# Optimization experiments

Measured on AMD Instinct MI355X. Metric: run time of the kernel, lower is better.

The kernel has to match this reference:

```python
import jax, jax.numpy as jnp
import numpy as np

B, L, D, N_NODE = 1024, 32, 128, 50000

def setup_inputs() -> dict:
    key = jax.random.key(0)
    ks = jax.random.split(key, 20)
    rn = lambda k, shape, s=0.05: (jax.random.normal(k, shape, jnp.float32) * s)
    return {
        "items": jax.random.randint(ks[0], (B, L), 0, N_NODE),
        "A_in": jax.random.uniform(ks[1], (B, L, L), jnp.float32),
        "A_out": jax.random.uniform(ks[2], (B, L, L), jnp.float32),
        "inter_item_emb": jax.random.normal(ks[3], (B, L, D), jnp.float32),
        "seq_len": jax.random.randint(ks[4], (B,), 1, L + 1),
        "emb_table": rn(ks[5], (N_NODE, D), 0.1),
        # GGNN propagation weights
        "W_in": rn(ks[6], (D, D)), "b_in": jnp.zeros((D,), jnp.float32),
        "W_out": rn(ks[7], (D, D)), "b_out": jnp.zeros((D,), jnp.float32),
        "W_a": rn(ks[8], (2 * D, 3 * D)),   # acts on concat(a_in, a_out)
        "U_h": rn(ks[9], (D, 3 * D)),       # acts on hidden state
        "b_gru": jnp.zeros((3 * D,), jnp.float32),
        # ItemFusing GRUCell (input=local/intra, hidden=global/inter)
        "Wi": rn(ks[10], (D, 3 * D)), "bi": jnp.zeros((3 * D,), jnp.float32),
        "Wh": rn(ks[11], (D, 3 * D)), "bh": jnp.zeros((3 * D,), jnp.float32),
        # get_final_s attention readout
        "W1": rn(ks[12], (D, D)), "b1": jnp.zeros((D,), jnp.float32),
        "W2": rn(ks[13], (D, D)), "b2": jnp.zeros((D,), jnp.float32),
        "wq": rn(ks[14], (D, 1)), "bq": jnp.zeros((1,), jnp.float32),
        "W3": rn(ks[15], (2 * D, D)), "b3": jnp.zeros((D,), jnp.float32),
    }

def _gru_gates(gi, gh, h_prev):
    # torch GRU(Cell) math: r,z,n gate order
    i_r, i_z, i_n = jnp.split(gi, 3, axis=-1)
    h_r, h_z, h_n = jnp.split(gh, 3, axis=-1)
    r = jax.nn.sigmoid(i_r + h_r)
    z = jax.nn.sigmoid(i_z + h_z)
    n = jnp.tanh(i_n + r * h_n)
    return (1.0 - z) * n + z * h_prev

def reference(items, A_in, A_out, inter_item_emb, seq_len, emb_table,
              W_in, b_in, W_out, b_out, W_a, U_h, b_gru,
              Wi, bi, Wh, bh, W1, b1, W2, b2, wq, bq, W3, b3):
    # --- embedding lookup: [B, L, D]
    h = emb_table[items]
    # --- GGNN propagation (1 step): adjacency matmul + GRU-gated update
    a_in = jnp.einsum('blm,bmd->bld', A_in, h @ W_in + b_in)
    a_out = jnp.einsum('blm,bmd->bld', A_out, h @ W_out + b_out)
    a = jnp.concatenate([a_in, a_out], axis=-1)          # [B, L, 2D]
    intra = _gru_gates(a @ W_a + b_gru, h @ U_h, h)       # [B, L, D]
    # --- ItemFusing: GRUCell(input=intra, hidden=inter)
    final = _gru_gates(intra @ Wi + bi, inter_item_emb @ Wh + bh, inter_item_emb)
    # --- get_final_s (session attention readout, padded/masked form)
    mask = (jnp.arange(L)[None, :] < seq_len[:, None]).astype(final.dtype)  # [B, L]
    v_n = final[jnp.arange(B), seq_len - 1]                                 # [B, D] last valid node
    gates = jax.nn.sigmoid((v_n @ W1 + b1)[:, None, :] + final @ W2 + b2)   # [B, L, D]
    alpha = gates @ wq + bq                                                 # [B, L, 1]
    s_g = jnp.sum(alpha * final * mask[:, :, None], axis=1)                 # [B, D]
    h_s = jnp.concatenate([v_n, s_g], axis=-1) @ W3 + b3                    # [B, D]
    # --- Embedding2Score (item_fusing branch): final_s @ emb.T
    scores = h_s @ emb_table.T                                              # [B, N_NODE]
    return scores
```

## Files before the change

kernel.cpp:

```cpp
#include <hip/hip_runtime.h>
#include <hip/hip_bf16.h>

#define L_SEQ 32
#define DIM 128
#define NN 50000

typedef __attribute__((ext_vector_type(8))) short bf16x8s;
typedef __attribute__((ext_vector_type(4))) float f32x4;

__device__ __forceinline__ float bf2f(short s){
    union{unsigned u; float f;} v; v.u = ((unsigned)(unsigned short)s) << 16; return v.f;
}
__device__ __forceinline__ short f2bf(float x){
    union{__hip_bfloat16 h; short s;} u; u.h = __float2bfloat16(x); return u.s;
}
__device__ __forceinline__ void ldf8(const float* p, float* w){
    const float4 a = *reinterpret_cast<const float4*>(p);
    const float4 b = *reinterpret_cast<const float4*>(p+4);
    w[0]=a.x; w[1]=a.y; w[2]=a.z; w[3]=a.w;
    w[4]=b.x; w[5]=b.y; w[6]=b.z; w[7]=b.w;
}
__device__ __forceinline__ void st8bf(short* dst, const float* v){
    union{ short s[8]; uint4 q; } u;
    #pragma unroll
    for (int i=0;i<8;++i) u.s[i] = f2bf(v[i]);
    *reinterpret_cast<uint4*>(dst) = u.q;
}
__device__ __forceinline__ bf16x8s cvt8(const float* v){
    union{ short s[8]; bf16x8s b; } u;
    #pragma unroll
    for (int i=0;i<8;++i) u.s[i] = f2bf(v[i]);
    return u.b;
}
__device__ __forceinline__ float sigmoidf(float x){ return 1.0f/(1.0f+__expf(-x)); }
__device__ __forceinline__ float tanh_fast(float x){
    x = fminf(fmaxf(x, -15.f), 15.f);
    float e = __expf(2.f*x);
    return (e-1.f)/(e+1.f);
}
__device__ __forceinline__ f32x4 mfma16(bf16x8s a, bf16x8s b, f32x4 c){
    return __builtin_amdgcn_mfma_f32_16x16x32_bf16(a, b, c, 0, 0, 0);
}

__global__ __launch_bounds__(256)
void prep_kernel(const float* __restrict__ W_in, const float* __restrict__ W_out,
                 const float* __restrict__ W_a,  const float* __restrict__ U_h,
                 const float* __restrict__ Wi,   const float* __restrict__ Wh,
                 const float* __restrict__ W1,   const float* __restrict__ W2,
                 const float* __restrict__ W3,   short* __restrict__ wt,
                 const float* __restrict__ emb,  short* __restrict__ embf)
{
    const int blk = blockIdx.x;
    if (blk < 1344) {
        int idx = blk*256 + threadIdx.x;
        const float* src; int Rm1, lR, C, local, off;
        if      (idx < 16384) { src=W_in;  local=idx;        off=0;      Rm1=127; lR=7; C=128; }
        else if (idx < 32768) { src=W_out; local=idx-16384;  off=16384;  Rm1=127; lR=7; C=128; }
        else if (idx < 131072){ src=W_a;   local=idx-32768;  off=32768;  Rm1=255; lR=8; C=384; }
        else if (idx < 180224){ src=U_h;   local=idx-131072; off=131072; Rm1=127; lR=7; C=384; }
        else if (idx < 229376){ src=Wi;    local=idx-180224; off=180224; Rm1=127; lR=7; C=384; }
        else if (idx < 278528){ src=Wh;    local=idx-229376; off=229376; Rm1=127; lR=7; C=384; }
        else if (idx < 294912){ src=W1;    local=idx-278528; off=278528; Rm1=127; lR=7; C=128; }
        else if (idx < 311296){ src=W2;    local=idx-294912; off=294912; Rm1=127; lR=7; C=128; }
        else if (idx < 344064){ src=W3;    local=idx-311296; off=311296; Rm1=255; lR=8; C=128; }
        else return;
        int r = local & Rm1;
        int c = local >> lR;
        wt[off + local] = f2bf(src[r*C + c]);
    } else {
        const size_t idx = ((size_t)(blk-1344)*256 + threadIdx.x) * 8;
        float v[8]; ldf8(emb + idx, v);
        st8bf(embf + idx, v);
    }
}

#define LDH 136
#define LDA 264
#define LDT 40

__global__ __launch_bounds__(256)
void graph_fused(const int* __restrict__ items,
                 const float* __restrict__ A_in, const float* __restrict__ A_out,
                 const float* __restrict__ inter,
                 const int* __restrict__ seq_len,
                 const float* __restrict__ emb,
                 const short* __restrict__ embf,
                 const float* __restrict__ b_in, const float* __restrict__ b_out,
                 const float* __restrict__ b_gru,
                 const float* __restrict__ bi, const float* __restrict__ bh,
                 const float* __restrict__ b1, const float* __restrict__ b2,
                 const float* __restrict__ wq, const float* __restrict__ bq,
                 const float* __restrict__ b3,
                 const short* __restrict__ wt,
                 short* __restrict__ hs_bf)
{
    const short* WinT  = wt + 0;
    const short* WoutT = wt + 16384;
    const short* WaT   = wt + 32768;
    const short* UhT   = wt + 131072;
    const short* WiT   = wt + 180224;
    const short* WhT   = wt + 229376;
    const short* W1T   = wt + 278528;
    const short* W2T   = wt + 294912;
    const short* W3T   = wt + 311296;

    __shared__ __align__(16) short s_h[32*LDH];
    __shared__ __align__(16) short s_a[32*LDA];
    __shared__ __align__(16) short s_r3[32*LDH];
    __shared__ __align__(16) short s_r4[2*32*LDH];

    short* s_Ain  = s_r3;
    short* s_Aout = s_r3 + 32*LDT;
    short* s_x    = s_r3;
    short* xT     = s_r4;
    short* s_int  = s_r4;
    short* s_fin  = s_r4 + 32*LDH;
    float* s_vn    = (float*)s_a;
    float* s_q1    = s_vn + 128;
    float* s_sg    = s_q1 + 128;
    float* s_red   = s_sg + 128;
    float* s_alpha = s_red + 256;

    const int b    = blockIdx.x;
    const int t    = threadIdx.x;
    const int wave = t >> 6;
    const int lane = t & 63;
    const int quad = lane >> 4;
    const int lc   = lane & 15;
    const int kq   = quad * 8;

    float pre_i[2][8];
    #pragma unroll
    for (int i=0;i<2;++i) {
        int c = t + i*256;
        int l = c >> 4, k = (c & 15) * 8;
        ldf8(inter + ((size_t)b*L_SEQ + l)*DIM + k, pre_i[i]);
    }
    if (embf) {
        #pragma unroll
        for (int i=0;i<2;++i) {
            int c = t + i*256;
            int l = c >> 4, k = (c & 15) * 8;
            int it = items[b*L_SEQ + l];
            *reinterpret_cast<uint4*>(&s_h[l*LDH + k]) =
                *reinterpret_cast<const uint4*>(embf + (size_t)it*DIM + k);
        }
    } else {
        #pragma unroll
        for (int i=0;i<2;++i) {
            int c = t + i*256;
            int l = c >> 4, k = (c & 15) * 8;
            int it = items[b*L_SEQ + l];
            float v[8]; ldf8(emb + (size_t)it*DIM + k, v);
            st8bf(&s_h[l*LDH + k], v);
        }
    }
    {
        const int which = t >> 7;
        const int rem   = t & 127;
        const int l = rem >> 2, m = (rem & 3) * 8;
        const float* src = which ? A_out : A_in;
        float v[8]; ldf8(src + b*L_SEQ*L_SEQ + l*L_SEQ + m, v);
        st8bf((which ? s_Aout : s_Ain) + l*LDT + m, v);
    }
    __syncthreads();

    #pragma unroll
    for (int op = 0; op < 2; ++op) {
        const short* WT_ = op ? WoutT : WinT;
        #pragma unroll
        for (int p = 0; p < 2; ++p) {
            const int nt = wave*2 + p;
            const int n  = nt*16 + lc;
            const float bv = op ? b_out[n] : b_in[n];
            f32x4 acc0 = {bv,bv,bv,bv}, acc1 = {bv,bv,bv,bv};
            #pragma unroll
            for (int ks = 0; ks < 4; ++ks) {
                const int ko = ks*32 + kq;
                bf16x8s bb = *(const bf16x8s*)(WT_ + n*128 + ko);
                bf16x8s a0 = *(const bf16x8s*)(&s_h[(lc   )*LDH + ko]);
                bf16x8s a1 = *(const bf16x8s*)(&s_h[(16+lc)*LDH + ko]);
                acc0 = mfma16(a0, bb, acc0);
                acc1 = mfma16(a1, bb, acc1);
            }
            union{short s[4]; unsigned long long q;} u0, u1;
            #pragma unroll
            for (int i=0;i<4;++i){ u0.s[i]=f2bf(acc0[i]); u1.s[i]=f2bf(acc1[i]); }
            *(unsigned long long*)(&xT[n*LDT + 0  + quad*4]) = u0.q;
            *(unsigned long long*)(&xT[n*LDT + 16 + quad*4]) = u1.q;
        }
        __syncthreads();
        const short* Abuf = op ? s_Aout : s_Ain;
        #pragma unroll
        for (int u = 0; u < 4; ++u) {
            int unit = wave*4 + u;
            int nt = unit >> 1, m0 = (unit & 1)*16;
            bf16x8s a  = *(const bf16x8s*)(&Abuf[(m0+lc)*LDT + kq]);
            bf16x8s bb = *(const bf16x8s*)(&xT[(nt*16+lc)*LDT + kq]);
            f32x4 acc = {0.f,0.f,0.f,0.f};
            acc = mfma16(a, bb, acc);
            #pragma unroll
            for (int i=0;i<4;++i)
                s_a[(m0+quad*4+i)*LDA + op*128 + nt*16 + lc] = f2bf(acc[i]);
        }
        __syncthreads();
    }

    #pragma unroll
    for (int i=0;i<2;++i) {
        int c = t + i*256;
        int l = c >> 4, k = (c & 15) * 8;
        st8bf(&s_int[l*LDH + k], pre_i[i]);
    }

    #pragma unroll
    for (int g = wave; g < 8; g += 4) {
        const int n = g*16 + lc;
        const float vr = b_gru[n], vz = b_gru[128+n], vn2 = b_gru[256+n];
        f32x4 ar[2], az[2], an[2], pr[2], pz[2], pn[2];
        #pragma unroll
        for (int m=0;m<2;++m){
            ar[m]=(f32x4){vr,vr,vr,vr}; az[m]=(f32x4){vz,vz,vz,vz}; an[m]=(f32x4){vn2,vn2,vn2,vn2};
            pr[m]=(f32x4){0,0,0,0}; pz[m]=pr[m]; pn[m]=pr[m];
        }
        #pragma unroll
        for (int ks=0; ks<8; ++ks) {
            const int ko = ks*32 + kq;
            bf16x8s br = *(const bf16x8s*)(WaT + (n      )*256 + ko);
            bf16x8s bz = *(const bf16x8s*)(WaT + (n + 128)*256 + ko);
            bf16x8s bn = *(const bf16x8s*)(WaT + (n + 256)*256 + ko);
            #pragma unroll
            for (int m=0;m<2;++m){
                bf16x8s a = *(const bf16x8s*)(&s_a[(m*16+lc)*LDA + ko]);
                ar[m]=mfma16(a,br,ar[m]); az[m]=mfma16(a,bz,az[m]); an[m]=mfma16(a,bn,an[m]);
            }
        }
        #pragma unroll
        for (int ks=0; ks<4; ++ks) {
            const int ko = ks*32 + kq;
            bf16x8s br = *(const bf16x8s*)(UhT + (n      )*128 + ko);
            bf16x8s bz = *(const bf16x8s*)(UhT + (n + 128)*128 + ko);
            bf16x8s bn = *(const bf16x8s*)(UhT + (n + 256)*128 + ko);
            #pragma unroll
            for (int m=0;m<2;++m){
                bf16x8s a = *(const bf16x8s*)(&s_h[(m*16+lc)*LDH + ko]);
                pr[m]=mfma16(a,br,pr[m]); pz[m]=mfma16(a,bz,pz[m]); pn[m]=mfma16(a,bn,pn[m]);
            }
        }
        #pragma unroll
        for (int m=0;m<2;++m)
        #pragma unroll
        for (int i=0;i<4;++i){
            const int row = m*16 + quad*4 + i;
            float hp = bf2f(s_h[row*LDH + n]);
            float r  = sigmoidf(ar[m][i] + pr[m][i]);
            float z  = sigmoidf(az[m][i] + pz[m][i]);
            float nn = tanh_fast(an[m][i] + r*pn[m][i]);
            s_x[row*LDH + n] = f2bf((1.f - z)*nn + z*hp);
        }
    }
    __syncthreads();

    #pragma unroll
    for (int g = wave; g < 8; g += 4) {
        const int n = g*16 + lc;
        const float vir = bi[n], viz = bi[128+n], vin = bi[256+n];
        const float vhr = bh[n], vhz = bh[128+n], vhn = bh[256+n];
        f32x4 ar[2], az[2], an[2], pr[2], pz[2], pn[2];
        #pragma unroll
        for (int m=0;m<2;++m){
            ar[m]=(f32x4){vir,vir,vir,vir}; az[m]=(f32x4){viz,viz,viz,viz}; an[m]=(f32x4){vin,vin,vin,vin};
            pr[m]=(f32x4){vhr,vhr,vhr,vhr}; pz[m]=(f32x4){vhz,vhz,vhz,vhz}; pn[m]=(f32x4){vhn,vhn,vhn,vhn};
        }
        #pragma unroll
        for (int ks=0; ks<4; ++ks) {
            const int ko = ks*32 + kq;
            bf16x8s br = *(const bf16x8s*)(WiT + (n      )*128 + ko);
            bf16x8s bz = *(const bf16x8s*)(WiT + (n + 128)*128 + ko);
            bf16x8s bn = *(const bf16x8s*)(WiT + (n + 256)*128 + ko);
            #pragma unroll
            for (int m=0;m<2;++m){
                bf16x8s a = *(const bf16x8s*)(&s_x[(m*16+lc)*LDH + ko]);
                ar[m]=mfma16(a,br,ar[m]); az[m]=mfma16(a,bz,az[m]); an[m]=mfma16(a,bn,an[m]);
            }
        }
        #pragma unroll
        for (int ks=0; ks<4; ++ks) {
            const int ko = ks*32 + kq;
            bf16x8s br = *(const bf16x8s*)(WhT + (n      )*128 + ko);
            bf16x8s bz = *(const bf16x8s*)(WhT + (n + 128)*128 + ko);
            bf16x8s bn = *(const bf16x8s*)(WhT + (n + 256)*128 + ko);
            #pragma unroll
            for (int m=0;m<2;++m){
                bf16x8s a = *(const bf16x8s*)(&s_int[(m*16+lc)*LDH + ko]);
                pr[m]=mfma16(a,br,pr[m]); pz[m]=mfma16(a,bz,pz[m]); pn[m]=mfma16(a,bn,pn[m]);
            }
        }
        #pragma unroll
        for (int m=0;m<2;++m)
        #pragma unroll
        for (int i=0;i<4;++i){
            const int row = m*16 + quad*4 + i;
            float hp = bf2f(s_int[row*LDH + n]);
            float r  = sigmoidf(ar[m][i] + pr[m][i]);
            float z  = sigmoidf(az[m][i] + pz[m][i]);
            float nn = tanh_fast(an[m][i] + r*pn[m][i]);
            s_fin[row*LDH + n] = f2bf((1.f - z)*nn + z*hp);
        }
    }
    __syncthreads();

    const int slen = seq_len[b];
    if (t < DIM) s_vn[t] = bf2f(s_fin[(slen-1)*LDH + t]);
    __syncthreads();
    if (t < DIM) {
        float acc = b1[t] + b2[t];
        #pragma unroll
        for (int k8=0; k8<16; ++k8) {
            union{ uint4 q; short s[8]; } u;
            u.q = *reinterpret_cast<const uint4*>(W1T + t*128 + k8*8);
            #pragma unroll
            for (int u2=0;u2<8;++u2) acc += s_vn[k8*8+u2]*bf2f(u.s[u2]);
        }
        s_q1[t] = acc;
    }
    __syncthreads();
    #pragma unroll
    for (int tl = wave; tl < 16; tl += 4) {
        const int m0 = (tl & 1)*16, nt = tl >> 1;
        const int n  = nt*16 + lc;
        f32x4 acc = {0.f,0.f,0.f,0.f};
        #pragma unroll
        for (int ks=0; ks<4; ++ks) {
            const int ko = ks*32 + kq;
            bf16x8s a  = *(const bf16x8s*)(&s_fin[(m0+lc)*LDH + ko]);
            bf16x8s bb = *(const bf16x8s*)(W2T + n*128 + ko);
            acc = mfma16(a, bb, acc);
        }
        const float qb  = s_q1[n];
        const float wqv = wq[n];
        float p[4];
        #pragma unroll
        for (int i=0;i<4;++i) p[i] = sigmoidf(acc[i] + qb) * wqv;
        #pragma unroll
        for (int off=1; off<16; off<<=1) {
            #pragma unroll
            for (int i=0;i<4;++i) p[i] += __shfl_xor(p[i], off);
        }
        if (lc == 0) {
            #pragma unroll
            for (int i=0;i<4;++i) s_red[(m0+quad*4+i)*8 + nt] = p[i];
        }
    }
    __syncthreads();
    if (t < L_SEQ) {
        float al = bq[0];
        #pragma unroll
        for (int u=0;u<8;++u) al += s_red[t*8+u];
        s_alpha[t] = (t < slen) ? al : 0.f;
    }
    __syncthreads();
    if (t < DIM) {
        float sg = 0.f;
        #pragma unroll
        for (int l=0;l<L_SEQ;++l) sg += s_alpha[l]*bf2f(s_fin[l*LDH + t]);
        s_sg[t] = sg;
    }
    __syncthreads();
    if (t < DIM) {
        float acc = b3[t];
        #pragma unroll
        for (int k8=0; k8<16; ++k8) {
            union{ uint4 q; short s[8]; } u;
            u.q = *reinterpret_cast<const uint4*>(W3T + t*256 + k8*8);
            #pragma unroll
            for (int u2=0;u2<8;++u2) acc += s_vn[k8*8+u2]*bf2f(u.s[u2]);
        }
        #pragma unroll
        for (int k8=0; k8<16; ++k8) {
            union{ uint4 q; short s[8]; } u;
            u.q = *reinterpret_cast<const uint4*>(W3T + t*256 + 128 + k8*8);
            #pragma unroll
            for (int u2=0;u2<8;++u2) acc += s_sg[k8*8+u2]*bf2f(u.s[u2]);
        }
        hs_bf[b*DIM + t] = f2bf(acc);
    }
}

__global__ __launch_bounds__(256)
void scores_bf(const short* __restrict__ hs, const short* __restrict__ embf,
               float* __restrict__ out)
{
    const int t    = threadIdx.x;
    const int wave = t >> 6;
    const int lane = t & 63;
    const int quad = lane >> 4;
    const int lc   = lane & 15;
    const int kq   = quad * 8;
    const int n0   = blockIdx.x * 64;
    const int mb   = blockIdx.y * 256 + wave*64;

    bf16x8s hf[4][4];
    #pragma unroll
    for (int mi=0; mi<4; ++mi)
        #pragma unroll
        for (int ks=0; ks<4; ++ks)
            hf[mi][ks] = *(const bf16x8s*)(hs + (size_t)(mb + mi*16 + lc)*DIM + ks*32 + kq);

    #pragma unroll
    for (int nt=0; nt<4; ++nt) {
        const int nr  = n0 + nt*16 + lc;
        const int nld = nr < NN ? nr : NN-1;
        bf16x8s ef[4];
        #pragma unroll
        for (int ks=0; ks<4; ++ks)
            ef[ks] = *(const bf16x8s*)(embf + (size_t)nld*DIM + ks*32 + kq);
        const int nbase = n0 + nt*16 + quad*4;
        #pragma unroll
        for (int mi=0; mi<4; ++mi) {
            f32x4 acc = {0.f,0.f,0.f,0.f};
            #pragma unroll
            for (int ks=0; ks<4; ++ks) acc = mfma16(ef[ks], hf[mi][ks], acc);
            if (nbase < NN) {
                __builtin_nontemporal_store(acc,
                    reinterpret_cast<f32x4*>(&out[(size_t)(mb + mi*16 + lc)*NN + nbase]));
            }
        }
    }
}

__global__ __launch_bounds__(256)
void scores_kernel(const short* __restrict__ hs, const float* __restrict__ emb,
                   float* __restrict__ out)
{
    const int t    = threadIdx.x;
    const int wave = t >> 6;
    const int lane = t & 63;
    const int quad = lane >> 4;
    const int lc   = lane & 15;
    const int kq   = quad * 8;
    const int n0   = blockIdx.x * 64;
    const int m0   = blockIdx.y * 64 + wave*16;

    bf16x8s af[4];
    #pragma unroll
    for (int ks=0; ks<4; ++ks)
        af[ks] = *(const bf16x8s*)(hs + (size_t)(m0 + lc)*DIM + ks*32 + kq);

    #pragma unroll
    for (int nt=0; nt<4; ++nt) {
        const int nabs = n0 + nt*16 + lc;
        const int nld  = nabs < NN ? nabs : NN-1;
        f32x4 acc = {0.f,0.f,0.f,0.f};
        #pragma unroll
        for (int ks=0; ks<4; ++ks) {
            float v[8]; ldf8(emb + (size_t)nld*DIM + ks*32 + kq, v);
            acc = mfma16(af[ks], cvt8(v), acc);
        }
        if (nabs < NN) {
            #pragma unroll
            for (int i=0;i<4;++i)
                out[(size_t)(m0 + quad*4 + i)*NN + nabs] = acc[i];
        }
    }
}

extern "C" void kernel_launch(void* const* d_in, const int* in_sizes, int n_in,
                              void* d_out, int out_size, void* d_ws, size_t ws_size,
                              hipStream_t stream)
{
    const int*   items   = (const int*)  d_in[0];
    const float* A_in    = (const float*)d_in[1];
    const float* A_out   = (const float*)d_in[2];
    const float* inter   = (const float*)d_in[3];
    const int*   seq_len = (const int*)  d_in[4];
    const float* emb     = (const float*)d_in[5];
    const float* W_in = (const float*)d_in[6],  *b_in  = (const float*)d_in[7];
    const float* W_out= (const float*)d_in[8],  *b_out = (const float*)d_in[9];
    const float* W_a  = (const float*)d_in[10], *U_h   = (const float*)d_in[11];
    const float* b_gru= (const float*)d_in[12];
    const float* Wi   = (const float*)d_in[13], *bi    = (const float*)d_in[14];
    const float* Wh   = (const float*)d_in[15], *bh    = (const float*)d_in[16];
    const float* W1   = (const float*)d_in[17], *b1    = (const float*)d_in[18];
    const float* W2   = (const float*)d_in[19], *b2    = (const float*)d_in[20];
    const float* wq   = (const float*)d_in[21], *bq    = (const float*)d_in[22];
    const float* W3   = (const float*)d_in[23], *b3    = (const float*)d_in[24];
    float* out = (float*)d_out;
    short* hs_bf = (short*)d_ws;
    short* wt    = (short*)((char*)d_ws + 262144);
    short* embf  = (short*)((char*)d_ws + 1048576);

    const size_t need_bf = 1048576 + (size_t)NN*DIM*2;
    const bool use_bf = (ws_size >= need_bf);

    prep_kernel<<<use_bf ? 4469 : 1344, 256, 0, stream>>>(
        W_in, W_out, W_a, U_h, Wi, Wh, W1, W2, W3, wt, emb, embf);
    graph_fused<<<1024, 256, 0, stream>>>(items, A_in, A_out, inter, seq_len, emb,
        use_bf ? embf : (const short*)nullptr,
        b_in, b_out, b_gru, bi, bh, b1, b2, wq, bq, b3, wt, hs_bf);
    if (use_bf)
        scores_bf<<<dim3(782, 4), 256, 0, stream>>>(hs_bf, embf, out);
    else
        scores_kernel<<<dim3(782, 16), 256, 0, stream>>>(hs_bf, emb, out);
}
```

Before: 402.7 us.

## Shrink graph kernel shared memory via aliasing and swizzle scores block order

The graph kernel's separate shared buffers are merged into one smaller aliased arena, with the intra-state store moved after the first GRU stage so regions can overlap. A launch bound of 4 blocks per CU is added to raise occupancy. Separately, the scores kernel now uses a 1D grid remapped so that the 4 row-blocks sharing an embedding tile run close together, improving L2 reuse of the embedding table. An extra barrier is added, and the register cap may cause spills.

```diff
diff --git a/kernel.cpp b/kernel.cpp
--- a/kernel.cpp
+++ b/kernel.cpp
@@ -78,7 +78,7 @@
 #define LDA 264
 #define LDT 40
 
-__global__ __launch_bounds__(256)
+__global__ __launch_bounds__(256, 4)
 void graph_fused(const int* __restrict__ items,
                  const float* __restrict__ A_in, const float* __restrict__ A_out,
                  const float* __restrict__ inter,
@@ -104,18 +104,16 @@
     const short* W2T   = wt + 294912;
     const short* W3T   = wt + 311296;
 
-    __shared__ __align__(16) short s_h[32*LDH];
-    __shared__ __align__(16) short s_a[32*LDA];
-    __shared__ __align__(16) short s_r3[32*LDH];
-    __shared__ __align__(16) short s_r4[2*32*LDH];
-
-    short* s_Ain  = s_r3;
-    short* s_Aout = s_r3 + 32*LDT;
-    short* s_x    = s_r3;
-    short* xT     = s_r4;
-    short* s_int  = s_r4;
-    short* s_fin  = s_r4 + 32*LDH;
-    float* s_vn    = (float*)s_a;
+    __shared__ __align__(16) short smem[20480];
+    short* s_h    = smem;
+    short* s_Ain  = smem + 4352;
+    short* s_Aout = smem + 5632;
+    short* xT     = smem + 6912;
+    short* s_a    = smem + 12032;
+    short* s_x    = smem + 4352;
+    short* s_int  = smem;
+    short* s_fin  = smem + 8704;
+    float* s_vn    = (float*)(smem + 13056);
     float* s_q1    = s_vn + 128;
     float* s_sg    = s_q1 + 128;
     float* s_red   = s_sg + 128;
@@ -207,13 +205,6 @@
     }
 
     #pragma unroll
-    for (int i=0;i<2;++i) {
-        int c = t + i*256;
-        int l = c >> 4, k = (c & 15) * 8;
-        st8bf(&s_int[l*LDH + k], pre_i[i]);
-    }
-
-    #pragma unroll
     for (int g = wave; g < 8; g += 4) {
         const int n = g*16 + lc;
         const float vr = b_gru[n], vz = b_gru[128+n], vn2 = b_gru[256+n];
@@ -262,6 +253,14 @@
     __syncthreads();
 
     #pragma unroll
+    for (int i=0;i<2;++i) {
+        int c = t + i*256;
+        int l = c >> 4, k = (c & 15) * 8;
+        st8bf(&s_int[l*LDH + k], pre_i[i]);
+    }
+    __syncthreads();
+
+    #pragma unroll
     for (int g = wave; g < 8; g += 4) {
         const int n = g*16 + lc;
         const float vir = bi[n], viz = bi[128+n], vin = bi[256+n];
@@ -391,14 +390,19 @@
 void scores_bf(const short* __restrict__ hs, const short* __restrict__ embf,
                float* __restrict__ out)
 {
+    const int bid  = blockIdx.x;
+    const int r    = bid & 7;
+    const int y    = (bid >> 3) & 3;
+    const int x    = (bid >> 5) * 8 + r;
+    if (x >= 782) return;
     const int t    = threadIdx.x;
     const int wave = t >> 6;
     const int lane = t & 63;
     const int quad = lane >> 4;
     const int lc   = lane & 15;
     const int kq   = quad * 8;
-    const int n0   = blockIdx.x * 64;
-    const int mb   = blockIdx.y * 256 + wave*64;
+    const int n0   = x * 64;
+    const int mb   = y * 256 + wave*64;
 
     bf16x8s hf[4][4];
     #pragma unroll
@@ -499,7 +503,7 @@
         use_bf ? embf : (const short*)nullptr,
         b_in, b_out, b_gru, bi, bh, b1, b2, wq, bq, b3, wt, hs_bf);
     if (use_bf)
-        scores_bf<<<dim3(782, 4), 256, 0, stream>>>(hs_bf, embf, out);
+        scores_bf<<<3136, 256, 0, stream>>>(hs_bf, embf, out);
     else
         scores_kernel<<<dim3(782, 16), 256, 0, stream>>>(hs_bf, emb, out);
 }
```

New measurement: 407.9 us. Within noise of the previous version (+1.3%).
